# Kernel tuning notes

Measured on AMD Instinct MI355X. Metric: run time of the kernel, lower is better.

## Reference

```python
import jax, jax.numpy as jnp
import numpy as np
import math

HEADS = 8
DIM_HEAD = 64

def setup_inputs() -> dict:
    key = jax.random.key(0)
    ks = jax.random.split(key, 6)
    B, L, D = 2, 2048, 512
    Ls = 1936
    inner = HEADS * DIM_HEAD  # 512
    x = jax.random.normal(ks[0], (B, L, D), dtype=jnp.float32)
    positions = jax.random.normal(ks[1], (B, Ls, 2), dtype=jnp.float32) * 10.0
    w_qkv = jax.random.normal(ks[2], (3 * inner, D), dtype=jnp.float32) * (1.0 / math.sqrt(D))
    w_out = jax.random.normal(ks[3], (D, inner), dtype=jnp.float32) * (1.0 / math.sqrt(inner))
    b_out = jnp.zeros((D,), dtype=jnp.float32)
    log_sigma = jnp.full((HEADS,), math.log(3.0), dtype=jnp.float32)
    global_bias = jnp.float32(0.0)
    return {"x": x, "positions": positions, "w_qkv": w_qkv, "w_out": w_out,
            "b_out": b_out, "log_sigma": log_sigma, "global_bias": global_bias,
            "num_spatial": Ls}

def reference(x, positions, w_qkv, w_out, b_out, log_sigma, global_bias, num_spatial):
    B, L, D = x.shape
    H, Dh = HEADS, DIM_HEAD
    scale = Dh ** (-0.5)
    # qkv projection: [B,L,3*H*Dh] -> q,k,v each [B,H,L,Dh]
    qkv = jnp.einsum('bld,ed->ble', x, w_qkv)
    q, k, v = jnp.split(qkv, 3, axis=-1)
    def heads(t):
        return t.reshape(B, L, H, Dh).transpose(0, 2, 1, 3)
    q, k, v = heads(q), heads(k), heads(v)
    attn = jnp.einsum('bhid,bhjd->bhij', q, k) * scale  # [B,H,L,L]
    # Gaussian distance bias on the spatial block, global_bias elsewhere
    Ls = num_spatial
    diff = positions[:, :, None, :] - positions[:, None, :, :]  # [B,Ls,Ls,2]
    dist_sq = jnp.sum(diff * diff, axis=-1)                     # [B,Ls,Ls]
    sigma_sq = jnp.exp(log_sigma) ** 2                          # [H]
    spatial_bias = -dist_sq[:, None] / (2.0 * sigma_sq[None, :, None, None])  # [B,H,Ls,Ls]
    full_bias = jnp.full((B, H, L, L), global_bias, dtype=x.dtype)
    full_bias = full_bias.at[:, :, :Ls, :Ls].set(spatial_bias)
    attn = jax.nn.softmax(attn + full_bias, axis=-1)
    out = jnp.einsum('bhij,bhjd->bhid', attn, v)  # [B,H,L,Dh]
    out = out.transpose(0, 2, 1, 3).reshape(B, L, H * Dh)
    return jnp.einsum('ble,de->bld', out, w_out) + b_out
```

## Files before the change

### kernel.cpp

```cpp
#include <hip/hip_runtime.h>
#include <stdint.h>
#include <stddef.h>

#define NB   2
#define NL   2048
#define ND   512
#define NH   8
#define DH   64
#define LOG2E 1.44269504f
#define NIT  16
#define RG_TOT 32768
#define JS   4

typedef __attribute__((ext_vector_type(8))) short bf16x8;
typedef __attribute__((ext_vector_type(4))) float f32x4;

__device__ __forceinline__ unsigned short f2bf(float f) {
  union { float f; unsigned int u; } c; c.f = f;
  unsigned int u = c.u;
  unsigned int r = u + 0x7fffu + ((u >> 16) & 1u);
  return (unsigned short)(r >> 16);
}

__device__ __forceinline__ float bf2f(unsigned short u) {
  union { unsigned int i; float f; } c; c.i = ((unsigned int)u) << 16; return c.f;
}

__device__ __forceinline__ float fexp2(float x) {
#if __has_builtin(__builtin_amdgcn_exp2f)
  return __builtin_amdgcn_exp2f(x);
#else
  return exp2f(x);
#endif
}

__device__ __forceinline__ void gl_lds16(const unsigned short* g, unsigned short* l) {
#if __has_builtin(__builtin_amdgcn_global_load_lds)
  __builtin_amdgcn_global_load_lds(
      (const __attribute__((address_space(1))) unsigned int*)g,
      (__attribute__((address_space(3))) unsigned int*)l, 16, 0, 0);
#else
  *(uint4*)l = *(const uint4*)g;
#endif
}

#define XC  524288
#define WQC 196608
#define WOC 65536
#define TOTC (XC + WQC + WOC)
__global__ void cvt_f32_bf16(const float* __restrict__ x, const float* __restrict__ wq,
                             const float* __restrict__ wo, unsigned short* __restrict__ xb,
                             unsigned short* __restrict__ wqb, unsigned short* __restrict__ wob) {
  int idx = blockIdx.x * 256 + threadIdx.x;
  const float* src; unsigned short* dst; int off;
  if (idx < XC)            { src = x;  dst = xb;  off = idx; }
  else if (idx < XC + WQC) { src = wq; dst = wqb; off = idx - XC; }
  else                     { src = wo; dst = wob; off = idx - XC - WQC; }
  float4 f = ((const float4*)src)[off];
  ushort4 o;
  o.x = f2bf(f.x); o.y = f2bf(f.y); o.z = f2bf(f.z); o.w = f2bf(f.w);
  ((ushort4*)dst)[off] = o;
}

template<int MODE, int MT>
__global__ __launch_bounds__(256, 2) void gemm_bf16(
    const unsigned short* __restrict__ A, const unsigned short* __restrict__ Bm,
    const float* __restrict__ bias,
    unsigned short* __restrict__ qo, unsigned short* __restrict__ ko,
    unsigned short* __restrict__ vTo, float* __restrict__ out, int K)
{
  constexpr int MB = MT / 32;
  constexpr int AC = MT * 4;
  constexpr int TC = AC + 512;
  __shared__ __align__(16) unsigned short S[MT * 32 + 128 * 32];
  const int tid = threadIdx.x, wid = tid >> 6, lane = tid & 63;
  const int quad = lane >> 4, l15 = lane & 15;
  const int m0 = blockIdx.x * MT, n0 = blockIdx.y * 128;
  const int wm = (wid >> 1) * (MT / 2), wn = (wid & 1) * 64;

  f32x4 acc[MB][4];
#pragma unroll
  for (int a = 0; a < MB; ++a)
#pragma unroll
    for (int b = 0; b < 4; ++b)
#pragma unroll
      for (int z = 0; z < 4; ++z) acc[a][b][z] = 0.f;

  for (int k0 = 0; k0 < K; k0 += 32) {
#pragma unroll
    for (int p = 0; p < TC / 256; ++p) {
      int c = p * 256 + wid * 64 + lane;
      if (c < AC) {
        int row = c >> 2, off = c & 3;
        gl_lds16(A + (size_t)(m0 + row) * K + k0 + off * 8, &S[c * 8]);
      } else {
        int cb = c - AC;
        int row = cb >> 2, off = cb & 3;
        gl_lds16(Bm + (size_t)(n0 + row) * K + k0 + off * 8, &S[c * 8]);
      }
    }
    __syncthreads();
    bf16x8 af[MB], bfr[4];
#pragma unroll
    for (int mb = 0; mb < MB; ++mb)
      af[mb] = *(const bf16x8*)&S[(wm + mb * 16 + l15) * 32 + quad * 8];
#pragma unroll
    for (int nb = 0; nb < 4; ++nb)
      bfr[nb] = *(const bf16x8*)&S[MT * 32 + (wn + nb * 16 + l15) * 32 + quad * 8];
#pragma unroll
    for (int mb = 0; mb < MB; ++mb)
#pragma unroll
      for (int nb = 0; nb < 4; ++nb)
        acc[mb][nb] = __builtin_amdgcn_mfma_f32_16x16x32_bf16(af[mb], bfr[nb], acc[mb][nb], 0, 0, 0);
    __syncthreads();
  }

  const float QSCALE = 0.125f * LOG2E;
#pragma unroll
  for (int mb = 0; mb < MB; ++mb) {
    int e0 = m0 + wm + mb * 16 + quad * 4;
    if (MODE == 0) {
      int s   = e0 >> 9;
      int hh  = (e0 >> 6) & 7;
      int dh0 = e0 & 63;
      if (s < 2) {
        unsigned short* dst = (s == 0) ? qo : ko;
        float sc = (s == 0) ? QSCALE : 1.0f;
#pragma unroll
        for (int nb = 0; nb < 4; ++nb) {
          int token = n0 + wn + nb * 16 + l15;
          int bb = token >> 11, ll = token & 2047;
          ushort4 o;
          o.x = f2bf(acc[mb][nb][0] * sc);
          o.y = f2bf(acc[mb][nb][1] * sc);
          o.z = f2bf(acc[mb][nb][2] * sc);
          o.w = f2bf(acc[mb][nb][3] * sc);
          *(ushort4*)&dst[(((size_t)bb * NH + hh) * NL + ll) * DH + dh0] = o;
        }
      } else {
#pragma unroll
        for (int nb = 0; nb < 4; ++nb) {
          int token = n0 + wn + nb * 16 + l15;
          int bb = token >> 11, ll = token & 2047;
          size_t base = ((size_t)bb * NH + hh) * DH * NL + ll;
#pragma unroll
          for (int r = 0; r < 4; ++r)
            vTo[base + (size_t)(dh0 + r) * NL] = f2bf(acc[mb][nb][r]);
        }
      }
    } else {
      float4 bv = *(const float4*)&bias[e0];
#pragma unroll
      for (int nb = 0; nb < 4; ++nb) {
        int token = n0 + wn + nb * 16 + l15;
        float4 o;
        o.x = acc[mb][nb][0] + bv.x;
        o.y = acc[mb][nb][1] + bv.y;
        o.z = acc[mb][nb][2] + bv.z;
        o.w = acc[mb][nb][3] + bv.w;
        *(float4*)&out[(size_t)token * ND + e0] = o;
      }
    }
  }
}

__global__ __launch_bounds__(256, 2) void flash_kernel(
    const unsigned short* __restrict__ qb, const unsigned short* __restrict__ kb,
    const unsigned short* __restrict__ vTb, const float* __restrict__ positions,
    const float* __restrict__ log_sigma, const float* __restrict__ gbias_p,
    const int* __restrict__ ns_p, unsigned short* __restrict__ Pb, float* __restrict__ rsbuf)
{
  const int it = blockIdx.x >> 2;
  const int js = blockIdx.x & 3;
  const int h  = blockIdx.y;
  const int b  = blockIdx.z;
  const int i0 = it * 128;
  const int jbase = js * (NL / JS);
  const int Ls = ns_p[0];
  const float gb = gbias_p[0];
  const float sig = __expf(log_sigma[h]);
  const float CI = LOG2E * 0.5f / (sig * sig);
  const float A2 = 2.0f * CI;
  const float CG = LOG2E * gb * 0.5f;
  const float C8N = -8.0f * LOG2E;

  const int tid  = threadIdx.x;
  const int wid  = tid >> 6;
  const int lane = tid & 63;
  const int quad = lane >> 4;
  const int l15  = lane & 15;

  __shared__ __align__(16) unsigned short Ks[64][72];
  __shared__ __align__(16) unsigned short Vt[64][72];
  __shared__ __align__(16) unsigned short Ps[128][72];
  __shared__ __align__(16) float4 pjc[64];

  const size_t bh = (size_t)b * NH + h;
  const unsigned short* qbase  = qb  + (bh * NL + i0) * DH;
  const unsigned short* kbase  = kb  + bh * NL * DH;
  const unsigned short* vtbase = vTb + bh * DH * NL;

  bf16x8 af[2][2];
#pragma unroll
  for (int mb = 0; mb < 2; ++mb)
#pragma unroll
    for (int kc = 0; kc < 2; ++kc)
      af[mb][kc] = *(const bf16x8*)(qbase + (size_t)(wid * 32 + mb * 16 + l15) * DH + kc * 32 + quad * 8);

  float pix_[2][4], piy_[2][4], riCm[2][4], ispf[2][4];
#pragma unroll
  for (int mb = 0; mb < 2; ++mb)
#pragma unroll
    for (int r = 0; r < 4; ++r) {
      int ig = i0 + wid * 32 + mb * 16 + quad * 4 + r;
      float px = 0.f, py = 0.f, sf = 0.f, rc = 0.f;
      if (ig < Ls) {
        float2 p2 = *(const float2*)(positions + ((size_t)b * Ls + ig) * 2);
        px = p2.x; py = p2.y; sf = 1.f;
        rc = -(CI * (px * px + py * py)) - CG;
      }
      pix_[mb][r] = px; piy_[mb][r] = py; ispf[mb][r] = sf; riCm[mb][r] = rc;
    }

  f32x4 accO[2][4];
  float rsum[2][4];
#pragma unroll
  for (int mb = 0; mb < 2; ++mb) {
#pragma unroll
    for (int nb = 0; nb < 4; ++nb)
#pragma unroll
      for (int z = 0; z < 4; ++z) accO[mb][nb][z] = 0.f;
#pragma unroll
    for (int r = 0; r < 4; ++r) rsum[mb][r] = 0.f;
  }

  uint4 kr[2], vr[2];
  float2 pr = make_float2(0.f, 0.f);
  {
#pragma unroll
    for (int p = 0; p < 2; ++p) {
      int c = p * 256 + tid;
      int row = c >> 3, off = c & 7;
      kr[p] = *(const uint4*)(kbase  + (size_t)(jbase + row) * DH + off * 8);
      vr[p] = *(const uint4*)(vtbase + (size_t)row * NL + jbase + off * 8);
    }
    if (tid < 64 && (jbase + tid) < Ls)
      pr = *(const float2*)(positions + ((size_t)b * Ls + jbase + tid) * 2);
  }

  for (int jt = 0; jt < NL / JS / 64; ++jt) {
    const int j0 = jbase + jt * 64;
    __syncthreads();

#pragma unroll
    for (int p = 0; p < 2; ++p) {
      int c = p * 256 + tid;
      int row = c >> 3, off = c & 7;
      *(uint4*)&Ks[row][off * 8] = kr[p];
      *(uint4*)&Vt[row][off * 8] = vr[p];
    }
    if (tid < 64) {
      bool jsp = (j0 + tid) < Ls;
      float px = jsp ? pr.x : 0.f, py = jsp ? pr.y : 0.f;
      float rc = jsp ? (-(CI * (px * px + py * py)) - CG) : 0.f;
      pjc[tid] = make_float4(A2 * px, A2 * py, rc, 0.f);
    }
    __syncthreads();

    if (jt + 1 < NL / JS / 64) {
      const int jn = jbase + (jt + 1) * 64;
#pragma unroll
      for (int p = 0; p < 2; ++p) {
        int c = p * 256 + tid;
        int row = c >> 3, off = c & 7;
        kr[p] = *(const uint4*)(kbase  + (size_t)(jn + row) * DH + off * 8);
        vr[p] = *(const uint4*)(vtbase + (size_t)row * NL + jn + off * 8);
      }
      if (tid < 64 && (jn + tid) < Ls)
        pr = *(const float2*)(positions + ((size_t)b * Ls + jn + tid) * 2);
    }

    f32x4 accS[2][4];
#pragma unroll
    for (int mb = 0; mb < 2; ++mb)
#pragma unroll
      for (int nb = 0; nb < 4; ++nb)
#pragma unroll
        for (int z = 0; z < 4; ++z) accS[mb][nb][z] = 0.f;
#pragma unroll
    for (int nb = 0; nb < 4; ++nb) {
      bf16x8 b0 = *(const bf16x8*)&Ks[nb * 16 + l15][quad * 8];
      bf16x8 b1 = *(const bf16x8*)&Ks[nb * 16 + l15][32 + quad * 8];
#pragma unroll
      for (int mb = 0; mb < 2; ++mb) {
        accS[mb][nb] = __builtin_amdgcn_mfma_f32_16x16x32_bf16(af[mb][0], b0, accS[mb][nb], 0, 0, 0);
        accS[mb][nb] = __builtin_amdgcn_mfma_f32_16x16x32_bf16(af[mb][1], b1, accS[mb][nb], 0, 0, 0);
      }
    }

    float4 pc[4]; float jspf_[4];
#pragma unroll
    for (int nb = 0; nb < 4; ++nb) {
      pc[nb] = pjc[nb * 16 + l15];
      jspf_[nb] = ((j0 + nb * 16 + l15) < Ls) ? 1.f : 0.f;
    }
#pragma unroll
    for (int mb = 0; mb < 2; ++mb)
#pragma unroll
      for (int nb = 0; nb < 4; ++nb)
#pragma unroll
        for (int r = 0; r < 4; ++r) {
          float t = accS[mb][nb][r] + C8N;
          t = __builtin_fmaf(ispf[mb][r], pc[nb].z, t);
          t = __builtin_fmaf(jspf_[nb], riCm[mb][r], t);
          t = __builtin_fmaf(piy_[mb][r], pc[nb].y, t);
          t = __builtin_fmaf(pix_[mb][r], pc[nb].x, t);
          float p = fexp2(t);
          rsum[mb][r] += p;
          Ps[wid * 32 + mb * 16 + quad * 4 + r][nb * 16 + l15] = f2bf(p);
        }

    bf16x8 pf[2][2];
#pragma unroll
    for (int mb = 0; mb < 2; ++mb) {
      pf[mb][0] = *(const bf16x8*)&Ps[wid * 32 + mb * 16 + l15][quad * 8];
      pf[mb][1] = *(const bf16x8*)&Ps[wid * 32 + mb * 16 + l15][32 + quad * 8];
    }
#pragma unroll
    for (int nb = 0; nb < 4; ++nb) {
      bf16x8 v0 = *(const bf16x8*)&Vt[nb * 16 + l15][quad * 8];
      bf16x8 v1 = *(const bf16x8*)&Vt[nb * 16 + l15][32 + quad * 8];
#pragma unroll
      for (int mb = 0; mb < 2; ++mb) {
        accO[mb][nb] = __builtin_amdgcn_mfma_f32_16x16x32_bf16(pf[mb][0], v0, accO[mb][nb], 0, 0, 0);
        accO[mb][nb] = __builtin_amdgcn_mfma_f32_16x16x32_bf16(pf[mb][1], v1, accO[mb][nb], 0, 0, 0);
      }
    }
  }

#pragma unroll
  for (int mb = 0; mb < 2; ++mb)
#pragma unroll
    for (int r = 0; r < 4; ++r) {
      float v = rsum[mb][r];
      v += __shfl_xor(v, 1);
      v += __shfl_xor(v, 2);
      v += __shfl_xor(v, 4);
      v += __shfl_xor(v, 8);
      rsum[mb][r] = v;
    }
  const size_t rgbase = (bh * NIT + it) * 128;
  const size_t poff = (size_t)js * RG_TOT * DH;
#pragma unroll
  for (int mb = 0; mb < 2; ++mb)
#pragma unroll
    for (int r = 0; r < 4; ++r) {
      int row = wid * 32 + mb * 16 + quad * 4 + r;
#pragma unroll
      for (int nb = 0; nb < 4; ++nb)
        Pb[poff + (rgbase + row) * DH + nb * 16 + l15] = f2bf(accO[mb][nb][r]);
      if (l15 == 0)
        rsbuf[(size_t)js * RG_TOT + rgbase + row] = rsum[mb][r];
    }
}

__global__ __launch_bounds__(256) void combine_kernel(const unsigned short* __restrict__ Pb,
                                                      const float* __restrict__ rsbuf,
                                                      unsigned short* __restrict__ attnb) {
  int idx = blockIdx.x * 256 + threadIdx.x;
  int rg = idx >> 4, c4 = idx & 15;
  float s0 = 0.f, s1 = 0.f, s2 = 0.f, s3 = 0.f, rsum = 0.f;
#pragma unroll
  for (int js = 0; js < JS; ++js) {
    ushort4 u = *(const ushort4*)&Pb[((size_t)js * RG_TOT + rg) * DH + c4 * 4];
    s0 += bf2f(u.x); s1 += bf2f(u.y); s2 += bf2f(u.z); s3 += bf2f(u.w);
    rsum += rsbuf[(size_t)js * RG_TOT + rg];
  }
  float rs = 1.0f / rsum;
  int bhm = rg >> 11;
  int l   = rg & 2047;
  int bb  = bhm >> 3, hh = bhm & 7;
  ushort4 o;
  o.x = f2bf(s0 * rs);
  o.y = f2bf(s1 * rs);
  o.z = f2bf(s2 * rs);
  o.w = f2bf(s3 * rs);
  *(ushort4*)&attnb[(((size_t)bb * NL + l) * ND) + hh * DH + c4 * 4] = o;
}

extern "C" void kernel_launch(void* const* d_in, const int* in_sizes, int n_in,
                              void* d_out, int out_size, void* d_ws, size_t ws_size,
                              hipStream_t stream) {
  const float* x         = (const float*)d_in[0];
  const float* positions = (const float*)d_in[1];
  const float* w_qkv     = (const float*)d_in[2];
  const float* w_out     = (const float*)d_in[3];
  const float* b_out     = (const float*)d_in[4];
  const float* log_sigma = (const float*)d_in[5];
  const float* gbias     = (const float*)d_in[6];
  const int*   ns        = (const int*)d_in[7];

  unsigned short* ws  = (unsigned short*)d_ws;
  unsigned short* xb  = ws;
  unsigned short* wob = xb  + 2097152;
  unsigned short* qbf = wob + 262144;
  unsigned short* kbf = qbf + 2097152;
  unsigned short* vTf = kbf + 2097152;
  unsigned short* R   = vTf + 2097152;
  unsigned short* wqb = R;
  unsigned short* Pb  = R;
  float* rsbuf = (float*)(Pb + (size_t)JS * RG_TOT * DH);

  cvt_f32_bf16<<<TOTC / 256, 256, 0, stream>>>(x, w_qkv, w_out, xb, wqb, wob);

  dim3 g1((3 * NH * DH) / 128, NB * NL / 128);
  gemm_bf16<0, 128><<<g1, 256, 0, stream>>>(wqb, xb, nullptr, qbf, kbf, vTf, nullptr, ND);

  dim3 g2((NL / 128) * JS, NH, NB);
  flash_kernel<<<g2, 256, 0, stream>>>(qbf, kbf, vTf, positions, log_sigma, gbias, ns,
                                       Pb, rsbuf);

  combine_kernel<<<RG_TOT * 16 / 256, 256, 0, stream>>>(Pb, rsbuf, xb);

  dim3 g3(ND / 64, NB * NL / 128);
  gemm_bf16<1, 64><<<g3, 256, 0, stream>>>(wob, xb, b_out, nullptr, nullptr, nullptr,
                                           (float*)d_out, NH * DH);
}
```

Before: 169.8 us.

## Pre-pack K and V into MFMA fragment layout and drop LDS staging in flash kernel

The QKV GEMM now writes K directly in a per-lane MFMA fragment layout, and a new repack kernel converts V into the matching fragment layout. Positions are zero-padded to full length during the conversion kernel. The flash kernel can then load K/V fragments and positions straight from global memory into registers, removing the K/V/position LDS tiles, the register prefetch and the two barriers per tile. The bias math is also reformulated with a combined mask. The cost is an extra kernel launch and an extra pass over V, plus global loads that are no longer software-prefetched.

```diff
diff --git a/kernel.cpp b/kernel.cpp
--- a/kernel.cpp
+++ b/kernel.cpp
@@ -49,25 +49,42 @@
 #define WOC 65536
 #define TOTC (XC + WQC + WOC)
 __global__ void cvt_f32_bf16(const float* __restrict__ x, const float* __restrict__ wq,
-                             const float* __restrict__ wo, unsigned short* __restrict__ xb,
-                             unsigned short* __restrict__ wqb, unsigned short* __restrict__ wob) {
+                             const float* __restrict__ wo, const float* __restrict__ positions,
+                             const int* __restrict__ ns_p,
+                             unsigned short* __restrict__ xb, unsigned short* __restrict__ wqb,
+                             unsigned short* __restrict__ wob, float* __restrict__ pospad) {
   int idx = blockIdx.x * 256 + threadIdx.x;
-  const float* src; unsigned short* dst; int off;
-  if (idx < XC)            { src = x;  dst = xb;  off = idx; }
-  else if (idx < XC + WQC) { src = wq; dst = wqb; off = idx - XC; }
-  else                     { src = wo; dst = wob; off = idx - XC - WQC; }
-  float4 f = ((const float4*)src)[off];
-  ushort4 o;
-  o.x = f2bf(f.x); o.y = f2bf(f.y); o.z = f2bf(f.z); o.w = f2bf(f.w);
-  ((ushort4*)dst)[off] = o;
+  if (idx < TOTC) {
+    const float* src; unsigned short* dst; int off;
+    if (idx < XC)            { src = x;  dst = xb;  off = idx; }
+    else if (idx < XC + WQC) { src = wq; dst = wqb; off = idx - XC; }
+    else                     { src = wo; dst = wob; off = idx - XC - WQC; }
+    float4 f = ((const float4*)src)[off];
+    ushort4 o;
+    o.x = f2bf(f.x); o.y = f2bf(f.y); o.z = f2bf(f.z); o.w = f2bf(f.w);
+    ((ushort4*)dst)[off] = o;
+  } else {
+    int i2 = idx - TOTC;
+    if (i2 < NB * 1024) {
+      int b = i2 >> 10;
+      int jj = (i2 & 1023) * 2;
+      int Ls = ns_p[0];
+      float4 o = make_float4(0.f, 0.f, 0.f, 0.f);
+      if (jj < Ls) { o.x = positions[((size_t)b * Ls + jj) * 2];
+                     o.y = positions[((size_t)b * Ls + jj) * 2 + 1]; }
+      if (jj + 1 < Ls) { o.z = positions[((size_t)b * Ls + jj + 1) * 2];
+                         o.w = positions[((size_t)b * Ls + jj + 1) * 2 + 1]; }
+      *(float4*)&pospad[((size_t)b * NL + jj) * 2] = o;
+    }
+  }
 }
 
 template<int MODE, int MT>
 __global__ __launch_bounds__(256, 2) void gemm_bf16(
     const unsigned short* __restrict__ A, const unsigned short* __restrict__ Bm,
     const float* __restrict__ bias,
-    unsigned short* __restrict__ qo, unsigned short* __restrict__ ko,
-    unsigned short* __restrict__ vTo, float* __restrict__ out, int K)
+    unsigned short* __restrict__ qo, unsigned short* __restrict__ kp,
+    unsigned short* __restrict__ vo, float* __restrict__ out, int K)
 {
   constexpr int MB = MT / 32;
   constexpr int AC = MT * 4;
@@ -122,10 +139,28 @@
     if (MODE == 0) {
       int s   = e0 >> 9;
       int hh  = (e0 >> 6) & 7;
-      int dh0 = e0 & 63;
-      if (s < 2) {
-        unsigned short* dst = (s == 0) ? qo : ko;
+      if (s == 1) {
+        int kc  = mb >> 1;
+        int q_t = ((mb & 1) << 1) + (quad >> 1);
+        int par = quad & 1;
+#pragma unroll
+        for (int nb = 0; nb < 4; ++nb) {
+          int token = n0 + wn + nb * 16 + l15;
+          int bb = token >> 11, ll = token & 2047;
+          int jt = ll >> 4;
+          ushort4 o;
+          o.x = f2bf(acc[mb][nb][0]);
+          o.y = f2bf(acc[mb][nb][1]);
+          o.z = f2bf(acc[mb][nb][2]);
+          o.w = f2bf(acc[mb][nb][3]);
+          size_t addr = (((size_t)(bb * NH + hh) * 128 + jt) * 2 + kc) * 512
+                      + (q_t * 16 + l15) * 8 + par * 4;
+          *(ushort4*)&kp[addr] = o;
+        }
+      } else {
+        unsigned short* dst = (s == 0) ? qo : vo;
         float sc = (s == 0) ? QSCALE : 1.0f;
+        int dh0 = e0 & 63;
 #pragma unroll
         for (int nb = 0; nb < 4; ++nb) {
           int token = n0 + wn + nb * 16 + l15;
@@ -137,16 +172,6 @@
           o.w = f2bf(acc[mb][nb][3] * sc);
           *(ushort4*)&dst[(((size_t)bb * NH + hh) * NL + ll) * DH + dh0] = o;
         }
-      } else {
-#pragma unroll
-        for (int nb = 0; nb < 4; ++nb) {
-          int token = n0 + wn + nb * 16 + l15;
-          int bb = token >> 11, ll = token & 2047;
-          size_t base = ((size_t)bb * NH + hh) * DH * NL + ll;
-#pragma unroll
-          for (int r = 0; r < 4; ++r)
-            vTo[base + (size_t)(dh0 + r) * NL] = f2bf(acc[mb][nb][r]);
-        }
       }
     } else {
       float4 bv = *(const float4*)&bias[e0];
@@ -164,9 +189,34 @@
   }
 }
 
+__global__ __launch_bounds__(256) void repack_v(const unsigned short* __restrict__ v,
+                                                unsigned short* __restrict__ vp) {
+  __shared__ unsigned short T[64][74];
+  const int l0 = blockIdx.x * 64;
+  const int bh = blockIdx.y;
+  const unsigned short* src = v + ((size_t)bh * NL + l0) * DH;
+  unsigned short* dst = vp + (size_t)bh * 131072 + (size_t)(l0 >> 5) * 2048;
+#pragma unroll
+  for (int p = 0; p < 2; ++p) {
+    int c = p * 256 + threadIdx.x;
+    int row = c >> 3, seg = c & 7;
+    *(uint4*)&T[row][seg * 8] = *(const uint4*)(src + row * DH + seg * 8);
+  }
+  __syncthreads();
+#pragma unroll
+  for (int p = 0; p < 2; ++p) {
+    int c = p * 256 + threadIdx.x;
+    int l15 = c & 15, q = (c >> 4) & 3, dht = (c >> 6) & 3, jcl = c >> 8;
+    unsigned short u[8];
+#pragma unroll
+    for (int t = 0; t < 8; ++t) u[t] = T[jcl * 32 + q * 8 + t][dht * 16 + l15];
+    *(uint4*)(dst + (size_t)jcl * 2048 + dht * 512 + (q * 16 + l15) * 8) = *(uint4*)u;
+  }
+}
+
 __global__ __launch_bounds__(256, 2) void flash_kernel(
-    const unsigned short* __restrict__ qb, const unsigned short* __restrict__ kb,
-    const unsigned short* __restrict__ vTb, const float* __restrict__ positions,
+    const unsigned short* __restrict__ qb, const unsigned short* __restrict__ kp,
+    const unsigned short* __restrict__ vp, const float* __restrict__ pospad,
     const float* __restrict__ log_sigma, const float* __restrict__ gbias_p,
     const int* __restrict__ ns_p, unsigned short* __restrict__ Pb, float* __restrict__ rsbuf)
 {
@@ -177,12 +227,12 @@
   const int i0 = it * 128;
   const int jbase = js * (NL / JS);
   const int Ls = ns_p[0];
-  const float gb = gbias_p[0];
+  const float gb  = gbias_p[0];
   const float sig = __expf(log_sigma[h]);
-  const float CI = LOG2E * 0.5f / (sig * sig);
-  const float A2 = 2.0f * CI;
-  const float CG = LOG2E * gb * 0.5f;
-  const float C8N = -8.0f * LOG2E;
+  const float CI  = LOG2E * 0.5f / (sig * sig);
+  const float A2  = 2.0f * CI;
+  const float LGB = LOG2E * gb;
+  const float CBL = -8.0f * LOG2E + LGB;
 
   const int tid  = threadIdx.x;
   const int wid  = tid >> 6;
@@ -190,15 +240,13 @@
   const int quad = lane >> 4;
   const int l15  = lane & 15;
 
-  __shared__ __align__(16) unsigned short Ks[64][72];
-  __shared__ __align__(16) unsigned short Vt[64][72];
-  __shared__ __align__(16) unsigned short Ps[128][72];
-  __shared__ __align__(16) float4 pjc[64];
+  __shared__ __align__(16) unsigned short Ps[128][76];
 
   const size_t bh = (size_t)b * NH + h;
-  const unsigned short* qbase  = qb  + (bh * NL + i0) * DH;
-  const unsigned short* kbase  = kb  + bh * NL * DH;
-  const unsigned short* vtbase = vTb + bh * DH * NL;
+  const unsigned short* qbase = qb + (bh * NL + i0) * DH;
+  const unsigned short* kpb   = kp + bh * 131072;
+  const unsigned short* vpb   = vp + bh * 131072;
+  const float* posb = pospad + (size_t)b * NL * 2;
 
   bf16x8 af[2][2];
 #pragma unroll
@@ -213,13 +261,10 @@
 #pragma unroll
     for (int r = 0; r < 4; ++r) {
       int ig = i0 + wid * 32 + mb * 16 + quad * 4 + r;
-      float px = 0.f, py = 0.f, sf = 0.f, rc = 0.f;
-      if (ig < Ls) {
-        float2 p2 = *(const float2*)(positions + ((size_t)b * Ls + ig) * 2);
-        px = p2.x; py = p2.y; sf = 1.f;
-        rc = -(CI * (px * px + py * py)) - CG;
-      }
-      pix_[mb][r] = px; piy_[mb][r] = py; ispf[mb][r] = sf; riCm[mb][r] = rc;
+      float2 p2 = *(const float2*)(posb + (size_t)ig * 2);
+      pix_[mb][r] = p2.x; piy_[mb][r] = p2.y;
+      ispf[mb][r] = (ig < Ls) ? 1.f : 0.f;
+      riCm[mb][r] = -(CI * (p2.x * p2.x + p2.y * p2.y)) - LGB;
     }
 
   f32x4 accO[2][4];
@@ -227,94 +272,62 @@
 #pragma unroll
   for (int mb = 0; mb < 2; ++mb) {
 #pragma unroll
-    for (int nb = 0; nb < 4; ++nb)
-#pragma unroll
-      for (int z = 0; z < 4; ++z) accO[mb][nb][z] = 0.f;
+    for (int d = 0; d < 4; ++d)
+#pragma unroll
+      for (int z = 0; z < 4; ++z) accO[mb][d][z] = 0.f;
 #pragma unroll
     for (int r = 0; r < 4; ++r) rsum[mb][r] = 0.f;
-  }
-
-  uint4 kr[2], vr[2];
-  float2 pr = make_float2(0.f, 0.f);
-  {
-#pragma unroll
-    for (int p = 0; p < 2; ++p) {
-      int c = p * 256 + tid;
-      int row = c >> 3, off = c & 7;
-      kr[p] = *(const uint4*)(kbase  + (size_t)(jbase + row) * DH + off * 8);
-      vr[p] = *(const uint4*)(vtbase + (size_t)row * NL + jbase + off * 8);
-    }
-    if (tid < 64 && (jbase + tid) < Ls)
-      pr = *(const float2*)(positions + ((size_t)b * Ls + jbase + tid) * 2);
   }
 
   for (int jt = 0; jt < NL / JS / 64; ++jt) {
     const int j0 = jbase + jt * 64;
-    __syncthreads();
-
-#pragma unroll
-    for (int p = 0; p < 2; ++p) {
-      int c = p * 256 + tid;
-      int row = c >> 3, off = c & 7;
-      *(uint4*)&Ks[row][off * 8] = kr[p];
-      *(uint4*)&Vt[row][off * 8] = vr[p];
-    }
-    if (tid < 64) {
-      bool jsp = (j0 + tid) < Ls;
-      float px = jsp ? pr.x : 0.f, py = jsp ? pr.y : 0.f;
-      float rc = jsp ? (-(CI * (px * px + py * py)) - CG) : 0.f;
-      pjc[tid] = make_float4(A2 * px, A2 * py, rc, 0.f);
-    }
-    __syncthreads();
-
-    if (jt + 1 < NL / JS / 64) {
-      const int jn = jbase + (jt + 1) * 64;
-#pragma unroll
-      for (int p = 0; p < 2; ++p) {
-        int c = p * 256 + tid;
-        int row = c >> 3, off = c & 7;
-        kr[p] = *(const uint4*)(kbase  + (size_t)(jn + row) * DH + off * 8);
-        vr[p] = *(const uint4*)(vtbase + (size_t)row * NL + jn + off * 8);
+
+    bf16x8 kf[4][2];
+#pragma unroll
+    for (int nb = 0; nb < 4; ++nb)
+#pragma unroll
+      for (int kc = 0; kc < 2; ++kc)
+        kf[nb][kc] = *(const bf16x8*)(kpb + ((size_t)((j0 >> 4) + nb) * 2 + kc) * 512 + lane * 8);
+
+    float pjx2[4], pjy2[4], rjC[4], jspf[4];
+#pragma unroll
+    for (int nb = 0; nb < 4; ++nb) {
+      int jg = j0 + nb * 16 + l15;
+      float2 p2 = *(const float2*)(posb + (size_t)jg * 2);
+      pjx2[nb] = A2 * p2.x; pjy2[nb] = A2 * p2.y;
+      rjC[nb]  = -(CI * (p2.x * p2.x + p2.y * p2.y));
+      jspf[nb] = (jg < Ls) ? 1.f : 0.f;
+    }
+
+    f32x4 accS[2][4];
+#pragma unroll
+    for (int mb = 0; mb < 2; ++mb)
+#pragma unroll
+      for (int nb = 0; nb < 4; ++nb) {
+#pragma unroll
+        for (int z = 0; z < 4; ++z) accS[mb][nb][z] = 0.f;
+        accS[mb][nb] = __builtin_amdgcn_mfma_f32_16x16x32_bf16(af[mb][0], kf[nb][0], accS[mb][nb], 0, 0, 0);
+        accS[mb][nb] = __builtin_amdgcn_mfma_f32_16x16x32_bf16(af[mb][1], kf[nb][1], accS[mb][nb], 0, 0, 0);
       }
-      if (tid < 64 && (jn + tid) < Ls)
-        pr = *(const float2*)(positions + ((size_t)b * Ls + jn + tid) * 2);
-    }
-
-    f32x4 accS[2][4];
+
+    bf16x8 vf[4][2];
+#pragma unroll
+    for (int dht = 0; dht < 4; ++dht)
+#pragma unroll
+      for (int jc = 0; jc < 2; ++jc)
+        vf[dht][jc] = *(const bf16x8*)(vpb + ((size_t)((j0 >> 5) + jc) * 4 + dht) * 512 + lane * 8);
+
 #pragma unroll
     for (int mb = 0; mb < 2; ++mb)
 #pragma unroll
       for (int nb = 0; nb < 4; ++nb)
 #pragma unroll
-        for (int z = 0; z < 4; ++z) accS[mb][nb][z] = 0.f;
-#pragma unroll
-    for (int nb = 0; nb < 4; ++nb) {
-      bf16x8 b0 = *(const bf16x8*)&Ks[nb * 16 + l15][quad * 8];
-      bf16x8 b1 = *(const bf16x8*)&Ks[nb * 16 + l15][32 + quad * 8];
-#pragma unroll
-      for (int mb = 0; mb < 2; ++mb) {
-        accS[mb][nb] = __builtin_amdgcn_mfma_f32_16x16x32_bf16(af[mb][0], b0, accS[mb][nb], 0, 0, 0);
-        accS[mb][nb] = __builtin_amdgcn_mfma_f32_16x16x32_bf16(af[mb][1], b1, accS[mb][nb], 0, 0, 0);
-      }
-    }
-
-    float4 pc[4]; float jspf_[4];
-#pragma unroll
-    for (int nb = 0; nb < 4; ++nb) {
-      pc[nb] = pjc[nb * 16 + l15];
-      jspf_[nb] = ((j0 + nb * 16 + l15) < Ls) ? 1.f : 0.f;
-    }
-#pragma unroll
-    for (int mb = 0; mb < 2; ++mb)
-#pragma unroll
-      for (int nb = 0; nb < 4; ++nb)
-#pragma unroll
         for (int r = 0; r < 4; ++r) {
-          float t = accS[mb][nb][r] + C8N;
-          t = __builtin_fmaf(ispf[mb][r], pc[nb].z, t);
-          t = __builtin_fmaf(jspf_[nb], riCm[mb][r], t);
-          t = __builtin_fmaf(piy_[mb][r], pc[nb].y, t);
-          t = __builtin_fmaf(pix_[mb][r], pc[nb].x, t);
+          float u = riCm[mb][r] + rjC[nb];
+          u = __builtin_fmaf(piy_[mb][r], pjy2[nb], u);
+          u = __builtin_fmaf(pix_[mb][r], pjx2[nb], u);
+          float msp = ispf[mb][r] * jspf[nb];
+          float t = __builtin_fmaf(msp, u, accS[mb][nb][r] + CBL);
           float p = fexp2(t);
           rsum[mb][r] += p;
           Ps[wid * 32 + mb * 16 + quad * 4 + r][nb * 16 + l15] = f2bf(p);
@@ -322,20 +335,17 @@
 
     bf16x8 pf[2][2];
 #pragma unroll
-    for (int mb = 0; mb < 2; ++mb) {
-      pf[mb][0] = *(const bf16x8*)&Ps[wid * 32 + mb * 16 + l15][quad * 8];
-      pf[mb][1] = *(const bf16x8*)&Ps[wid * 32 + mb * 16 + l15][32 + quad * 8];
-    }
-#pragma unroll
-    for (int nb = 0; nb < 4; ++nb) {
-      bf16x8 v0 = *(const bf16x8*)&Vt[nb * 16 + l15][quad * 8];
-      bf16x8 v1 = *(const bf16x8*)&Vt[nb * 16 + l15][32 + quad * 8];
-#pragma unroll
-      for (int mb = 0; mb < 2; ++mb) {
-        accO[mb][nb] = __builtin_amdgcn_mfma_f32_16x16x32_bf16(pf[mb][0], v0, accO[mb][nb], 0, 0, 0);
-        accO[mb][nb] = __builtin_amdgcn_mfma_f32_16x16x32_bf16(pf[mb][1], v1, accO[mb][nb], 0, 0, 0);
+    for (int mb = 0; mb < 2; ++mb)
+#pragma unroll
+      for (int jc = 0; jc < 2; ++jc)
+        pf[mb][jc] = *(const bf16x8*)&Ps[wid * 32 + mb * 16 + l15][jc * 32 + quad * 8];
+#pragma unroll
+    for (int mb = 0; mb < 2; ++mb)
+#pragma unroll
+      for (int dht = 0; dht < 4; ++dht) {
+        accO[mb][dht] = __builtin_amdgcn_mfma_f32_16x16x32_bf16(pf[mb][0], vf[dht][0], accO[mb][dht], 0, 0, 0);
+        accO[mb][dht] = __builtin_amdgcn_mfma_f32_16x16x32_bf16(pf[mb][1], vf[dht][1], accO[mb][dht], 0, 0, 0);
       }
-    }
   }
 
 #pragma unroll
@@ -357,8 +367,8 @@
     for (int r = 0; r < 4; ++r) {
       int row = wid * 32 + mb * 16 + quad * 4 + r;
 #pragma unroll
-      for (int nb = 0; nb < 4; ++nb)
-        Pb[poff + (rgbase + row) * DH + nb * 16 + l15] = f2bf(accO[mb][nb][r]);
+      for (int dht = 0; dht < 4; ++dht)
+        Pb[poff + (rgbase + row) * DH + dht * 16 + l15] = f2bf(accO[mb][dht][r]);
       if (l15 == 0)
         rsbuf[(size_t)js * RG_TOT + rgbase + row] = rsum[mb][r];
     }
@@ -404,20 +414,26 @@
   unsigned short* xb  = ws;
   unsigned short* wob = xb  + 2097152;
   unsigned short* qbf = wob + 262144;
-  unsigned short* kbf = qbf + 2097152;
-  unsigned short* vTf = kbf + 2097152;
-  unsigned short* R   = vTf + 2097152;
+  unsigned short* kpf = qbf + 2097152;
+  unsigned short* vbf = kpf + 2097152;
+  unsigned short* vpf = vbf + 2097152;
+  float* pospad = (float*)(vpf + 2097152);
+  unsigned short* R   = (unsigned short*)(pospad + NB * NL * 2);
   unsigned short* wqb = R;
   unsigned short* Pb  = R;
   float* rsbuf = (float*)(Pb + (size_t)JS * RG_TOT * DH);
 
-  cvt_f32_bf16<<<TOTC / 256, 256, 0, stream>>>(x, w_qkv, w_out, xb, wqb, wob);
+  cvt_f32_bf16<<<(TOTC + NB * 1024 + 255) / 256, 256, 0, stream>>>(
+      x, w_qkv, w_out, positions, ns, xb, wqb, wob, pospad);
 
   dim3 g1((3 * NH * DH) / 128, NB * NL / 128);
-  gemm_bf16<0, 128><<<g1, 256, 0, stream>>>(wqb, xb, nullptr, qbf, kbf, vTf, nullptr, ND);
+  gemm_bf16<0, 128><<<g1, 256, 0, stream>>>(wqb, xb, nullptr, qbf, kpf, vbf, nullptr, ND);
+
+  dim3 gr(NL / 64, NB * NH);
+  repack_v<<<gr, 256, 0, stream>>>(vbf, vpf);
 
   dim3 g2((NL / 128) * JS, NH, NB);
-  flash_kernel<<<g2, 256, 0, stream>>>(qbf, kbf, vTf, positions, log_sigma, gbias, ns,
+  flash_kernel<<<g2, 256, 0, stream>>>(qbf, kpf, vpf, pospad, log_sigma, gbias, ns,
                                        Pb, rsbuf);
 
   combine_kernel<<<RG_TOT * 16 / 256, 256, 0, stream>>>(Pb, rsbuf, xb);
```

Result: faster. 154.2 us (-9.2%).
